# Optimization experiments

Hardware: AMD Instinct MI355X
Metric: run time of the kernel (lower is better)

The kernel has to match this reference:

```python
import jax, jax.numpy as jnp
import numpy as np

B, T, ENC, DEC = 512, 500, 1024, 1024

def setup_inputs() -> dict:
    key = jax.random.key(0)
    k1, k2, k3, k4 = jax.random.split(key, 4)
    decoderFeature = jax.random.normal(k1, (B, DEC), dtype=jnp.float32)
    encoderFeature = jax.random.normal(k2, (B, T, ENC), dtype=jnp.float32)
    skill_net_lengths = jax.random.randint(k3, (B,), 1, T + 1, dtype=jnp.int32)
    W = jax.random.normal(k4, (ENC, DEC), dtype=jnp.float32) * (6.0 / (ENC + DEC)) ** 0.5
    return {"decoderFeature": decoderFeature, "encoderFeature": encoderFeature,
            "skill_net_lengths": skill_net_lengths, "W": W}

def reference(decoderFeature, encoderFeature, skill_net_lengths, W):
    # subResult = F.linear(decoderFeature, W) -> [B, ENC]
    sub = decoderFeature @ W.T
    # attn scores: bmm([B,1,ENC], [B,ENC,T]) -> [B, T]
    scores = jnp.einsum('be,bte->bt', sub, encoderFeature)
    valid = jnp.arange(T)[None, :] < skill_net_lengths[:, None]  # [B, T]
    scores = jnp.where(valid, scores, -jnp.inf)
    attn = jax.nn.softmax(scores, axis=-1)  # [B, T]
    sumResult = jnp.einsum('bt,bte->be', attn, encoderFeature)  # [B, ENC]
    return attn[:, None, :], sumResult
```

## Files before the change

### kernel.cpp

```cpp
#include <hip/hip_runtime.h>
#include <math.h>

#define B 512
#define T 500
#define ENC 1024
#define DEC 1024

#define GM 32
#define GN 64
#define GK 16

__global__ __launch_bounds__(256) void gemm_sub(
    const float* __restrict__ A,
    const float* __restrict__ Wm,
    float* __restrict__ C)
{
    __shared__ float As[GK][GM + 2];
    __shared__ float Bs[GK][GN + 4];

    const int tid = threadIdx.x;
    const int bm0 = blockIdx.y * GM;
    const int bn0 = blockIdx.x * GN;

    const int tx = tid & 15;
    const int ty = tid >> 4;

    float accr[2][4] = {{0.f,0.f,0.f,0.f},{0.f,0.f,0.f,0.f}};

    const int arow = tid >> 3;
    const int acol = (tid & 7) * 2;
    const int brow = tid >> 2;
    const int bcol = (tid & 3) * 4;

    for (int k0 = 0; k0 < DEC; k0 += GK) {
        float2 a2 = *(const float2*)(A + (size_t)(bm0 + arow) * DEC + k0 + acol);
        As[acol][arow]     = a2.x;
        As[acol + 1][arow] = a2.y;
        float4 b4 = *(const float4*)(Wm + (size_t)(bn0 + brow) * DEC + k0 + bcol);
        Bs[bcol][brow]     = b4.x;
        Bs[bcol + 1][brow] = b4.y;
        Bs[bcol + 2][brow] = b4.z;
        Bs[bcol + 3][brow] = b4.w;
        __syncthreads();
#pragma unroll
        for (int k = 0; k < GK; k++) {
            float2 av = *(const float2*)&As[k][ty * 2];
            float4 bv = *(const float4*)&Bs[k][tx * 4];
            accr[0][0] = fmaf(av.x, bv.x, accr[0][0]);
            accr[0][1] = fmaf(av.x, bv.y, accr[0][1]);
            accr[0][2] = fmaf(av.x, bv.z, accr[0][2]);
            accr[0][3] = fmaf(av.x, bv.w, accr[0][3]);
            accr[1][0] = fmaf(av.y, bv.x, accr[1][0]);
            accr[1][1] = fmaf(av.y, bv.y, accr[1][1]);
            accr[1][2] = fmaf(av.y, bv.z, accr[1][2]);
            accr[1][3] = fmaf(av.y, bv.w, accr[1][3]);
        }
        __syncthreads();
    }

    float4 c0 = make_float4(accr[0][0], accr[0][1], accr[0][2], accr[0][3]);
    float4 c1 = make_float4(accr[1][0], accr[1][1], accr[1][2], accr[1][3]);
    *(float4*)(C + (size_t)(bm0 + ty * 2) * ENC + bn0 + tx * 4)     = c0;
    *(float4*)(C + (size_t)(bm0 + ty * 2 + 1) * ENC + bn0 + tx * 4) = c1;
}

#define NW 8
#define BLK (NW * 64)

__global__ __launch_bounds__(BLK, 4) void attn_fused(
    const float* __restrict__ sub,
    const float* __restrict__ enc,
    const int* __restrict__ lens,
    float* __restrict__ out_attn,
    float* __restrict__ out_sum)
{
    __shared__ float lds_scores[T];
    __shared__ float lds_m[NW];
    __shared__ float lds_l[NW];
    __shared__ float lds_o[NW][ENC];

    const int b    = blockIdx.x;
    const int tid  = threadIdx.x;
    const int wave = tid >> 6;
    const int lane = tid & 63;
    const int len  = lens[b];

    const float* encb = enc + (size_t)b * T * ENC;
    const float* subb = sub + (size_t)b * ENC;

    float sub_r[16];
#pragma unroll
    for (int c = 0; c < 4; c++) {
        float4 s4 = *(const float4*)(subb + c * 256 + 4 * lane);
        sub_r[c * 4 + 0] = s4.x; sub_r[c * 4 + 1] = s4.y;
        sub_r[c * 4 + 2] = s4.z; sub_r[c * 4 + 3] = s4.w;
    }

    float acc[16];
#pragma unroll
    for (int i = 0; i < 16; i++) acc[i] = 0.f;
    float m = -INFINITY;
    float l = 0.f;

    int t = wave;
    float er[16];
    if (t < len) {
        const float* p = encb + (size_t)t * ENC + 4 * lane;
#pragma unroll
        for (int c = 0; c < 4; c++) {
            float4 v = *(const float4*)(p + c * 256);
            er[c * 4 + 0] = v.x; er[c * 4 + 1] = v.y;
            er[c * 4 + 2] = v.z; er[c * 4 + 3] = v.w;
        }
    }

    while (t < len) {
        const int tn = t + NW;
        float ern[16];
        if (tn < len) {
            const float* p = encb + (size_t)tn * ENC + 4 * lane;
#pragma unroll
            for (int c = 0; c < 4; c++) {
                float4 v = *(const float4*)(p + c * 256);
                ern[c * 4 + 0] = v.x; ern[c * 4 + 1] = v.y;
                ern[c * 4 + 2] = v.z; ern[c * 4 + 3] = v.w;
            }
        }

        float d = 0.f;
#pragma unroll
        for (int i = 0; i < 16; i++) d = fmaf(er[i], sub_r[i], d);
#pragma unroll
        for (int off = 32; off > 0; off >>= 1) d += __shfl_xor(d, off, 64);

        if (lane == 0) lds_scores[t] = d;

        if (d > m) {
            float alpha = __expf(m - d);
            l = l * alpha + 1.f;
#pragma unroll
            for (int i = 0; i < 16; i++) acc[i] = acc[i] * alpha + er[i];
            m = d;
        } else {
            float p = __expf(d - m);
            l += p;
#pragma unroll
            for (int i = 0; i < 16; i++) acc[i] = fmaf(p, er[i], acc[i]);
        }

        t = tn;
#pragma unroll
        for (int i = 0; i < 16; i++) er[i] = ern[i];
    }

    if (lane == 0) { lds_m[wave] = m; lds_l[wave] = l; }
#pragma unroll
    for (int c = 0; c < 4; c++) {
        float4 v = make_float4(acc[c * 4 + 0], acc[c * 4 + 1],
                               acc[c * 4 + 2], acc[c * 4 + 3]);
        *(float4*)&lds_o[wave][c * 256 + 4 * lane] = v;
    }
    __syncthreads();

    float mg = -INFINITY;
#pragma unroll
    for (int w = 0; w < NW; w++) mg = fmaxf(mg, lds_m[w]);
    float scale[NW];
    float lg = 0.f;
#pragma unroll
    for (int w = 0; w < NW; w++) {
        float mw = lds_m[w];
        float s  = (mw == -INFINITY) ? 0.f : __expf(mw - mg);
        scale[w] = s;
        lg = fmaf(lds_l[w], s, lg);
    }
    const float inv_l = 1.f / lg;

    const int e0 = 2 * tid;
    float o0 = 0.f, o1 = 0.f;
#pragma unroll
    for (int w = 0; w < NW; w++) {
        o0 = fmaf(scale[w], lds_o[w][e0], o0);
        o1 = fmaf(scale[w], lds_o[w][e0 + 1], o1);
    }
    *(float2*)(out_sum + (size_t)b * ENC + e0) = make_float2(o0 * inv_l, o1 * inv_l);

    for (int tt = tid; tt < T; tt += BLK) {
        float v = 0.f;
        if (tt < len) v = __expf(lds_scores[tt] - mg) * inv_l;
        out_attn[(size_t)b * T + tt] = v;
    }
}

extern "C" void kernel_launch(void* const* d_in, const int* in_sizes, int n_in,
                              void* d_out, int out_size, void* d_ws, size_t ws_size,
                              hipStream_t stream) {
    const float* dec  = (const float*)d_in[0];
    const float* enc  = (const float*)d_in[1];
    const int*   lens = (const int*)d_in[2];
    const float* Wm   = (const float*)d_in[3];

    float* out       = (float*)d_out;
    float* out_attn  = out;
    float* out_sum   = out + (size_t)B * T;
    float* sub       = (float*)d_ws;

    gemm_sub<<<dim3(16, 16), 256, 0, stream>>>(dec, Wm, sub);
    attn_fused<<<dim3(B), BLK, 0, stream>>>(sub, enc, lens, out_attn, out_sum);
}
```

Before: 1.280 ms.

## Process two encoder rows per wave step and prefetch GEMM tiles into registers

```diff
diff --git a/kernel.cpp b/kernel.cpp
--- a/kernel.cpp
+++ b/kernel.cpp
@@ -32,16 +32,26 @@
     const int brow = tid >> 2;
     const int bcol = (tid & 3) * 4;
 
+    const float* aptr = A  + (size_t)(bm0 + arow) * DEC + acol;
+    const float* bptr = Wm + (size_t)(bn0 + brow) * DEC + bcol;
+
+    float2 a2 = *(const float2*)(aptr);
+    float4 b4 = *(const float4*)(bptr);
+
     for (int k0 = 0; k0 < DEC; k0 += GK) {
-        float2 a2 = *(const float2*)(A + (size_t)(bm0 + arow) * DEC + k0 + acol);
         As[acol][arow]     = a2.x;
         As[acol + 1][arow] = a2.y;
-        float4 b4 = *(const float4*)(Wm + (size_t)(bn0 + brow) * DEC + k0 + bcol);
         Bs[bcol][brow]     = b4.x;
         Bs[bcol + 1][brow] = b4.y;
         Bs[bcol + 2][brow] = b4.z;
         Bs[bcol + 3][brow] = b4.w;
         __syncthreads();
+
+        if (k0 + GK < DEC) {
+            a2 = *(const float2*)(aptr + k0 + GK);
+            b4 = *(const float4*)(bptr + k0 + GK);
+        }
+
 #pragma unroll
         for (int k = 0; k < GK; k++) {
             float2 av = *(const float2*)&As[k][ty * 2];
@@ -67,6 +77,70 @@
 #define NW 8
 #define BLK (NW * 64)
 
+#define LOADROW(E, TT) do {                                            \
+    const float* _p = encb + (size_t)(TT) * ENC + 4 * lane;            \
+    float4 _v0 = *(const float4*)(_p);                                 \
+    float4 _v1 = *(const float4*)(_p + 256);                           \
+    float4 _v2 = *(const float4*)(_p + 512);                           \
+    float4 _v3 = *(const float4*)(_p + 768);                           \
+    E[0]=_v0.x;  E[1]=_v0.y;  E[2]=_v0.z;  E[3]=_v0.w;                 \
+    E[4]=_v1.x;  E[5]=_v1.y;  E[6]=_v1.z;  E[7]=_v1.w;                 \
+    E[8]=_v2.x;  E[9]=_v2.y;  E[10]=_v2.z; E[11]=_v2.w;                \
+    E[12]=_v3.x; E[13]=_v3.y; E[14]=_v3.z; E[15]=_v3.w;                \
+} while (0)
+
+#define LOADPAIR(E0, E1, TT) do {                                      \
+    LOADROW(E0, TT);                                                   \
+    if ((TT) + 1 < len) LOADROW(E1, (TT) + 1);                         \
+} while (0)
+
+#define PROCESS_PAIR(E0, E1, TT) do {                                  \
+    const bool _r1 = ((TT) + 1 < len);                                 \
+    if (!_r1) {                                                        \
+        _Pragma("unroll")                                              \
+        for (int _i = 0; _i < 16; _i++) E1[_i] = 0.f;                  \
+    }                                                                  \
+    float _d0a = 0.f, _d0b = 0.f, _d1a = 0.f, _d1b = 0.f;              \
+    _Pragma("unroll")                                                  \
+    for (int _i = 0; _i < 16; _i += 2) {                               \
+        _d0a = fmaf(E0[_i],     sub_r[_i],     _d0a);                  \
+        _d0b = fmaf(E0[_i + 1], sub_r[_i + 1], _d0b);                  \
+        _d1a = fmaf(E1[_i],     sub_r[_i],     _d1a);                  \
+        _d1b = fmaf(E1[_i + 1], sub_r[_i + 1], _d1b);                  \
+    }                                                                  \
+    float _d0 = _d0a + _d0b;                                           \
+    float _d1 = _d1a + _d1b;                                           \
+    _Pragma("unroll")                                                  \
+    for (int _off = 32; _off > 0; _off >>= 1) {                        \
+        _d0 += __shfl_xor(_d0, _off, 64);                              \
+        _d1 += __shfl_xor(_d1, _off, 64);                              \
+    }                                                                  \
+    if (lane == 0) {                                                   \
+        lds_scores[(TT)] = _d0;                                        \
+        if (_r1) lds_scores[(TT) + 1] = _d1;                           \
+    }                                                                  \
+    const float _d1e = _r1 ? _d1 : -INFINITY;                          \
+    const float _md  = fmaxf(_d0, _d1e);                               \
+    if (_md > m) {                                                     \
+        const float _al = __expf(m - _md);          \
+        const float _p0 = __expf(_d0 - _md);                           \
+        const float _p1 = _r1 ? __expf(_d1 - _md) : 0.f;               \
+        l = fmaf(l, _al, _p0 + _p1);                                   \
+        _Pragma("unroll")                                              \
+        for (int _i = 0; _i < 16; _i++)                                \
+            acc[_i] = fmaf(acc[_i], _al,                               \
+                           fmaf(_p0, E0[_i], _p1 * E1[_i]));           \
+        m = _md;                                                       \
+    } else {                                                           \
+        const float _p0 = __expf(_d0 - m);                             \
+        const float _p1 = _r1 ? __expf(_d1 - m) : 0.f;                 \
+        l += _p0 + _p1;                                                \
+        _Pragma("unroll")                                              \
+        for (int _i = 0; _i < 16; _i++)                                \
+            acc[_i] = fmaf(_p1, E1[_i], fmaf(_p0, E0[_i], acc[_i]));   \
+    }                                                                  \
+} while (0)
+
 __global__ __launch_bounds__(BLK, 4) void attn_fused(
     const float* __restrict__ sub,
     const float* __restrict__ enc,
@@ -102,55 +176,23 @@
     float m = -INFINITY;
     float l = 0.f;
 
-    int t = wave;
-    float er[16];
+    int t = 2 * wave;
     if (t < len) {
-        const float* p = encb + (size_t)t * ENC + 4 * lane;
-#pragma unroll
-        for (int c = 0; c < 4; c++) {
-            float4 v = *(const float4*)(p + c * 256);
-            er[c * 4 + 0] = v.x; er[c * 4 + 1] = v.y;
-            er[c * 4 + 2] = v.z; er[c * 4 + 3] = v.w;
+        float eA0[16], eA1[16], eB0[16], eB1[16];
+        LOADPAIR(eA0, eA1, t);
+        for (;;) {
+            const int tB = t + 2 * NW;
+            const bool vB = (tB < len);
+            if (vB) LOADPAIR(eB0, eB1, tB);
+            PROCESS_PAIR(eA0, eA1, t);
+            if (!vB) break;
+            const int tA = tB + 2 * NW;
+            const bool vA = (tA < len);
+            if (vA) LOADPAIR(eA0, eA1, tA);
+            PROCESS_PAIR(eB0, eB1, tB);
+            if (!vA) break;
+            t = tA;
         }
-    }
-
-    while (t < len) {
-        const int tn = t + NW;
-        float ern[16];
-        if (tn < len) {
-            const float* p = encb + (size_t)tn * ENC + 4 * lane;
-#pragma unroll
-            for (int c = 0; c < 4; c++) {
-                float4 v = *(const float4*)(p + c * 256);
-                ern[c * 4 + 0] = v.x; ern[c * 4 + 1] = v.y;
-                ern[c * 4 + 2] = v.z; ern[c * 4 + 3] = v.w;
-            }
-        }
-
-        float d = 0.f;
-#pragma unroll
-        for (int i = 0; i < 16; i++) d = fmaf(er[i], sub_r[i], d);
-#pragma unroll
-        for (int off = 32; off > 0; off >>= 1) d += __shfl_xor(d, off, 64);
-
-        if (lane == 0) lds_scores[t] = d;
-
-        if (d > m) {
-            float alpha = __expf(m - d);
-            l = l * alpha + 1.f;
-#pragma unroll
-            for (int i = 0; i < 16; i++) acc[i] = acc[i] * alpha + er[i];
-            m = d;
-        } else {
-            float p = __expf(d - m);
-            l += p;
-#pragma unroll
-            for (int i = 0; i < 16; i++) acc[i] = fmaf(p, er[i], acc[i]);
-        }
-
-        t = tn;
-#pragma unroll
-        for (int i = 0; i < 16; i++) er[i] = ern[i];
     }
 
     if (lane == 0) { lds_m[wave] = m; lds_l[wave] = l; }
```

New measurement: 1.260 ms. Within noise of the previous version (-1.5%).
